# Kernel optimization log

Measured on AMD Instinct MI355X. Metric: run time of the kernel, lower is better.

The kernel has to match this reference:

```python
import jax, jax.numpy as jnp
import numpy as np


def setup_inputs() -> dict:
    key = jax.random.key(0)
    k1, k2 = jax.random.split(key)
    B, F, Ci, R = 16, 1024, 64, 1
    Co, K = 64, 4
    ll = jax.random.normal(k1, (B, F, Ci, R), dtype=jnp.float32)
    logits = jax.random.normal(k2, (Co, Ci, K, K, R), dtype=jnp.float32)
    return {"ll": ll, "logits": logits}


def reference(ll, logits):
    # ll: (B, F, Ci, R)   logits: (Co, Ci, K, K, R)
    B, F, Ci, R = ll.shape
    Co, _, K, _, _ = logits.shape
    H = W = int(F ** 0.5)
    OH, OW = H // K, W // K
    # normalize weights over input channels (sum_dim=1)
    lw = jax.nn.log_softmax(logits, axis=1)  # (Co, Ci, K, K, R)
    # b (h w) ci r -> b ci h w r
    x = ll.reshape(B, H, W, Ci, R).transpose(0, 3, 1, 2, 4)
    # b ci (oh kh) (ow kw) r -> b ci oh ow kh kw r
    x = x.reshape(B, Ci, OH, K, OW, K, R).transpose(0, 1, 2, 4, 3, 5, 6)
    # broadcast-add log-weights (shared over oh, ow) then logsumexp over ci
    weighted = x[:, None] + lw[None, :, :, None, None, :, :, :]  # (B, Co, Ci, OH, OW, K, K, R)
    res = jax.scipy.special.logsumexp(weighted, axis=2)          # (B, Co, OH, OW, K, K, R)
    # b co oh ow kh kw r -> b (oh kh ow kw) co r
    out = res.transpose(0, 2, 4, 3, 5, 1, 6).reshape(B, F, Co, R)
    return out
```

## Files before the change

### kernel.cpp

```cpp
#include <hip/hip_runtime.h>

#define CI 64
#define CO 64
#define F_ 1024
#define KK 4
#define NPAT 16

__device__ __forceinline__ float bcast(float v, int l) {
    return __int_as_float(__builtin_amdgcn_readlane(__float_as_int(v), l));
}

__global__ __launch_bounds__(256) void prep_kernel(
    const float* __restrict__ logits, float* __restrict__ E)
{
    const int pat = blockIdx.x >> 2;
    const int q   = blockIdx.x & 3;
    const int t   = threadIdx.x;
    const int co  = t & 63;
    const int i   = t >> 6;
    #pragma unroll
    for (int k = 0; k < 4; ++k) {
        const int ci = q * 16 + i * 4 + k;
        const float e = __expf(logits[co * (CI * KK * KK) + ci * (KK * KK) + pat]);
        E[pat * (CI * CO) + (ci >> 2) * (CO * 4) + co * 4 + (ci & 3)] = e;
    }
}

__global__ __launch_bounds__(256, 4) void main_kernel(
    const float* __restrict__ ll, const float* __restrict__ E,
    float* __restrict__ out)
{
    const int tid   = threadIdx.x;
    const int lane  = tid & 63;
    const int wv    = tid >> 6;
    const int bid   = blockIdx.x;
    const int pat   = bid & (NPAT - 1);
    const int chunk = bid >> 4;
    const int kh = pat >> 2, kw = pat & 3;

    int   idx[4];
    float p[4];
    #pragma unroll
    for (int j = 0; j < 4; ++j) {
        const int pr = (chunk << 4) + (wv << 2) + j;
        const int b  = pr >> 6;
        const int oh = (pr >> 3) & 7;
        const int ow = pr & 7;
        const int f  = (oh * 4 + kh) * 32 + (ow * 4 + kw);
        idx[j] = (b * F_ + f) * CI + lane;
        p[j]   = ll[idx[j]];
    }

    float4 wv4[16];
    const float4* Ep4 = reinterpret_cast<const float4*>(E + pat * (CI * CO)) + lane;
    #pragma unroll
    for (int g = 0; g < 16; ++g) wv4[g] = Ep4[g * CO];
    float wreg[CI];
    #pragma unroll
    for (int g = 0; g < 16; ++g) {
        wreg[4 * g + 0] = wv4[g].x; wreg[4 * g + 1] = wv4[g].y;
        wreg[4 * g + 2] = wv4[g].z; wreg[4 * g + 3] = wv4[g].w;
    }

    float ts[8];
    #pragma unroll
    for (int i = 0; i < 8; ++i)
        ts[i] = (wreg[i] + wreg[i + 8]) + (wreg[i + 16] + wreg[i + 24])
              + (wreg[i + 32] + wreg[i + 40]) + (wreg[i + 48] + wreg[i + 56]);
    const float lsum = __logf(((ts[0] + ts[1]) + (ts[2] + ts[3]))
                            + ((ts[4] + ts[5]) + (ts[6] + ts[7])));

    #pragma unroll
    for (int j = 0; j < 4; ++j) p[j] = __expf(p[j]);

    float a0[4] = {0.f,0.f,0.f,0.f}, a1[4] = {0.f,0.f,0.f,0.f};
    float a2[4] = {0.f,0.f,0.f,0.f}, a3[4] = {0.f,0.f,0.f,0.f};
    #pragma unroll
    for (int ci = 0; ci < CI; ci += 4) {
        #pragma unroll
        for (int j = 0; j < 4; ++j) {
            a0[j] = fmaf(bcast(p[j], ci + 0), wreg[ci + 0], a0[j]);
            a1[j] = fmaf(bcast(p[j], ci + 1), wreg[ci + 1], a1[j]);
            a2[j] = fmaf(bcast(p[j], ci + 2), wreg[ci + 2], a2[j]);
            a3[j] = fmaf(bcast(p[j], ci + 3), wreg[ci + 3], a3[j]);
        }
    }
    #pragma unroll
    for (int j = 0; j < 4; ++j)
        out[idx[j]] = __logf((a0[j] + a1[j]) + (a2[j] + a3[j])) - lsum;
}

extern "C" void kernel_launch(void* const* d_in, const int* in_sizes, int n_in,
                              void* d_out, int out_size, void* d_ws, size_t ws_size,
                              hipStream_t stream) {
    const float* ll     = (const float*)d_in[0];
    const float* logits = (const float*)d_in[1];
    float* out = (float*)d_out;
    float* E   = (float*)d_ws;
    prep_kernel<<<dim3(64), dim3(256), 0, stream>>>(logits, E);
    main_kernel<<<dim3(1024), dim3(256), 0, stream>>>(ll, E, out);
}
```

Before: 64.06 us.

## Fuse weight exp prep into main kernel with bf16 shared-memory weights

Result: slower. 70.72 us (+10.4%).

```diff
diff --git a/kernel.cpp b/kernel.cpp
--- a/kernel.cpp
+++ b/kernel.cpp
@@ -3,46 +3,37 @@
 #define CI 64
 #define CO 64
 #define F_ 1024
-#define KK 4
-#define NPAT 16
 
 __device__ __forceinline__ float bcast(float v, int l) {
     return __int_as_float(__builtin_amdgcn_readlane(__float_as_int(v), l));
 }
 
-__global__ __launch_bounds__(256) void prep_kernel(
-    const float* __restrict__ logits, float* __restrict__ E)
-{
-    const int pat = blockIdx.x >> 2;
-    const int q   = blockIdx.x & 3;
-    const int t   = threadIdx.x;
-    const int co  = t & 63;
-    const int i   = t >> 6;
-    #pragma unroll
-    for (int k = 0; k < 4; ++k) {
-        const int ci = q * 16 + i * 4 + k;
-        const float e = __expf(logits[co * (CI * KK * KK) + ci * (KK * KK) + pat]);
-        E[pat * (CI * CO) + (ci >> 2) * (CO * 4) + co * 4 + (ci & 3)] = e;
-    }
+__device__ __forceinline__ unsigned int bf16_rne(float x) {
+    const unsigned int u = __float_as_uint(x);
+    return (u + 0x7fffu + ((u >> 16) & 1u)) >> 16;
 }
 
-__global__ __launch_bounds__(256, 4) void main_kernel(
-    const float* __restrict__ ll, const float* __restrict__ E,
+__global__ __launch_bounds__(512, 4) void fused_kernel(
+    const float* __restrict__ ll, const float* __restrict__ logits,
     float* __restrict__ out)
 {
+    __shared__ unsigned int Wb[8][32][64];
+
     const int tid   = threadIdx.x;
     const int lane  = tid & 63;
     const int wv    = tid >> 6;
     const int bid   = blockIdx.x;
-    const int pat   = bid & (NPAT - 1);
-    const int chunk = bid >> 4;
+    const int half  = bid & 1;
+    const int chunk = bid >> 1;
+
+    const int pat = half * 8 + wv;
     const int kh = pat >> 2, kw = pat & 3;
 
     int   idx[4];
     float p[4];
     #pragma unroll
     for (int j = 0; j < 4; ++j) {
-        const int pr = (chunk << 4) + (wv << 2) + j;
+        const int pr = chunk * 4 + j;
         const int b  = pr >> 6;
         const int oh = (pr >> 3) & 7;
         const int ow = pr & 7;
@@ -51,15 +42,33 @@
         p[j]   = ll[idx[j]];
     }
 
-    float4 wv4[16];
-    const float4* Ep4 = reinterpret_cast<const float4*>(E + pat * (CI * CO)) + lane;
-    #pragma unroll
-    for (int g = 0; g < 16; ++g) wv4[g] = Ep4[g * CO];
+    {
+        const float* base = logits + lane * (CI * 16) + half * 8;
+        #pragma unroll
+        for (int cc = 0; cc < 8; cc += 2) {
+            const int ci0 = 8 * wv + cc;
+            const float4 A = *reinterpret_cast<const float4*>(base + ci0 * 16);
+            const float4 Bv = *reinterpret_cast<const float4*>(base + ci0 * 16 + 4);
+            const float4 Cv = *reinterpret_cast<const float4*>(base + ci0 * 16 + 16);
+            const float4 D = *reinterpret_cast<const float4*>(base + ci0 * 16 + 20);
+            const float ea[8] = {A.x, A.y, A.z, A.w, Bv.x, Bv.y, Bv.z, Bv.w};
+            const float eb[8] = {Cv.x, Cv.y, Cv.z, Cv.w, D.x, D.y, D.z, D.w};
+            #pragma unroll
+            for (int pl = 0; pl < 8; ++pl) {
+                const unsigned int lo = bf16_rne(__expf(ea[pl]));
+                const unsigned int hi = bf16_rne(__expf(eb[pl]));
+                Wb[pl][4 * wv + (cc >> 1)][lane] = lo | (hi << 16);
+            }
+        }
+    }
+    __syncthreads();
+
     float wreg[CI];
     #pragma unroll
-    for (int g = 0; g < 16; ++g) {
-        wreg[4 * g + 0] = wv4[g].x; wreg[4 * g + 1] = wv4[g].y;
-        wreg[4 * g + 2] = wv4[g].z; wreg[4 * g + 3] = wv4[g].w;
+    for (int g = 0; g < 32; ++g) {
+        const unsigned int u = Wb[wv][g][lane];
+        wreg[2 * g]     = __uint_as_float(u << 16);
+        wreg[2 * g + 1] = __uint_as_float(u & 0xffff0000u);
     }
 
     float ts[8];
@@ -96,7 +105,5 @@
     const float* ll     = (const float*)d_in[0];
     const float* logits = (const float*)d_in[1];
     float* out = (float*)d_out;
-    float* E   = (float*)d_ws;
-    prep_kernel<<<dim3(64), dim3(256), 0, stream>>>(logits, E);
-    main_kernel<<<dim3(1024), dim3(256), 0, stream>>>(ll, E, out);
+    fused_kernel<<<dim3(512), dim3(512), 0, stream>>>(ll, logits, out);
 }
```
